# Kernel optimization log

Hardware: AMD Instinct MI355X
Metric: run time of the kernel (lower is better)

## Reference

```python
import jax, jax.numpy as jnp
import numpy as np
from jax import lax

B, N, C = 16, 2048, 128
NPOINT = 512
RADII = (0.1, 0.2, 0.4)
NSAMPLES = (16, 32, 48)
C_IN = C + 3          # use_xyz: relative xyz concatenated to features
C_OUT = 128
C_MID = C_OUT // 4    # mapping_func1 out channels (non-first-layer)


def fps(xyz, npoint):
    # sequential furthest point sampling; first index is 0 (matches CUDA FPS)
    b, n, _ = xyz.shape
    def step(carry, _):
        dist, last = carry
        p = xyz[jnp.arange(b), last]                    # (B,3) last selected point
        d = jnp.sum((xyz - p[:, None, :]) ** 2, -1)     # (B,N)
        dist = jnp.minimum(dist, d)
        nxt = jnp.argmax(dist, -1).astype(jnp.int32)
        return (dist, nxt), nxt
    idx0 = jnp.zeros((b,), jnp.int32)
    (_, _), rest = lax.scan(step, (jnp.full((b, n), 1e10, jnp.float32), idx0), None, length=npoint - 1)
    return jnp.concatenate([idx0[None], rest], 0).T     # (B,npoint)


def ball_query(xyz, new_xyz, radius, nsample):
    # first `nsample` in-ball indices (in original point order), pad with first hit
    n = xyz.shape[1]
    d2 = jnp.sum((new_xyz[:, :, None, :] - xyz[:, None, :, :]) ** 2, -1)  # (B,np,N)
    scores = jnp.where(d2 < radius * radius, jnp.arange(n, dtype=jnp.int32), n)
    vals = -lax.top_k(-scores, nsample)[0]               # ascending valid indices, invalid == n
    first = vals[..., :1]                                # center is always in its own ball
    return jnp.where(vals >= n, first, vals)             # (B,np,ns) int32


def gather_points(pts, idx):
    # pts (B,N,D), idx (B,np,ns) -> (B,np,ns,D)
    return jax.vmap(lambda p, i: p[i])(pts, idx)


def sa_forward(xyz, features, W1, b1, W2, b2, Wcr, bcr):
    fi = fps(xyz, NPOINT)
    new_xyz = jax.vmap(lambda p, i: p[i])(xyz, fi)       # (B,np,3)
    featT = jnp.transpose(features, (0, 2, 1))           # (B,N,C)
    outs = []
    for r, ns in zip(RADII, NSAMPLES):
        idx = ball_query(xyz, new_xyz, r, ns)
        g_xyz = gather_points(xyz, idx)                  # (B,np,ns,3) absolute neighbor coords
        rel = g_xyz - new_xyz[:, :, None, :]             # relative coords
        gf = gather_points(featT, idx)                   # (B,np,ns,C)
        x = jnp.concatenate([rel, gf], -1)               # (B,np,ns,C_in)
        dist = jnp.linalg.norm(rel, axis=-1, keepdims=True)
        ci = jnp.broadcast_to(new_xyz[:, :, None, :], g_xyz.shape)
        h10 = jnp.concatenate([dist, ci, g_xyz, rel], -1)        # relation prior (B,np,ns,10)
        h = jax.nn.relu(h10 @ W1 + b1) @ W2 + b2                 # dynamic weights (B,np,ns,C_in)
        pooled = jnp.max(jax.nn.relu(h * x), 2)                  # (B,np,C_in) max over neighbors
        outs.append(jax.nn.relu(pooled @ Wcr + bcr))             # channel raising (B,np,C_out)
    new_features = jnp.transpose(jnp.concatenate(outs, -1), (0, 2, 1))  # (B, 3*C_out, np)
    return new_xyz, new_features


def setup_inputs() -> dict:
    key = jax.random.key(0)
    ks = jax.random.split(key, 6)
    s = 0.05
    xyz = jax.random.uniform(ks[0], (B, N, 3), jnp.float32)
    features = jax.random.normal(ks[1], (B, C, N), jnp.float32)
    W1 = jax.random.normal(ks[2], (10, C_MID), jnp.float32) * s
    b1 = jnp.zeros((C_MID,), jnp.float32)
    W2 = jax.random.normal(ks[3], (C_MID, C_IN), jnp.float32) * s
    b2 = jnp.zeros((C_IN,), jnp.float32)
    Wcr = jax.random.normal(ks[4], (C_IN, C_OUT), jnp.float32) * s
    bcr = jnp.zeros((C_OUT,), jnp.float32)
    return dict(xyz=xyz, features=features, W1=W1, b1=b1, W2=W2, b2=b2, Wcr=Wcr, bcr=bcr)


def reference(xyz, features, W1, b1, W2, b2, Wcr, bcr):
    return sa_forward(xyz, features, W1, b1, W2, b2, Wcr, bcr)
```

## Files before the change

### kernel.cpp

```cpp
#include <hip/hip_runtime.h>
#include <hip/hip_bf16.h>

#define BATCH   16
#define NPTS    2048
#define NPOINT  512
#define CFEAT   128
#define CIN     131
#define CMID    32
#define NS_TOT  96
#define NTRANS  (BATCH * 256)
#define NCENT   (NPOINT * BATCH)
#define SMEM_BYTES 26688

typedef float v2f __attribute__((ext_vector_type(2)));

__device__ __forceinline__ float d2_rn(float ax, float ay, float az,
                                       float bx, float by, float bz) {
  float dx = __fsub_rn(ax, bx), dy = __fsub_rn(ay, by), dz = __fsub_rn(az, bz);
  return __fadd_rn(__fadd_rn(__fmul_rn(dx, dx), __fmul_rn(dy, dy)), __fmul_rn(dz, dz));
}

__device__ __forceinline__ unsigned long long wave_kmax64(unsigned long long k) {
#define KSTEP(CTRL, RMASK, BMASK)                                              \
  {                                                                            \
    unsigned hi = (unsigned)(k >> 32), lo = (unsigned)k;                       \
    unsigned thi = (unsigned)__builtin_amdgcn_update_dpp(                      \
        (int)hi, (int)hi, CTRL, RMASK, BMASK, false);                          \
    unsigned tlo = (unsigned)__builtin_amdgcn_update_dpp(                      \
        (int)lo, (int)lo, CTRL, RMASK, BMASK, false);                          \
    unsigned long long tk = ((unsigned long long)thi << 32) | tlo;             \
    k = tk > k ? tk : k;                                                       \
  }
  KSTEP(0x111, 0xf, 0xf)
  KSTEP(0x112, 0xf, 0xf)
  KSTEP(0x114, 0xf, 0xe)
  KSTEP(0x118, 0xf, 0xc)
  KSTEP(0x142, 0xa, 0xf)
  KSTEP(0x143, 0xc, 0xf)
#undef KSTEP
  return k;
}

__device__ __forceinline__ void fps_body(
    const float* __restrict__ xyz, float* __restrict__ out_xyz,
    int* prog, int b, int t, char* smem)
{
  __builtin_amdgcn_s_setprio(3);
  float* slx = (float*)smem;
  float* sly = (float*)(smem + 8192);
  float* slz = (float*)(smem + 16384);
  unsigned long long* skey = (unsigned long long*)(smem + 24576);
  int* slast = (int*)(smem + 24640);

  const float* xb = xyz + (size_t)b * NPTS * 3;
  for (int n = t; n < NPTS; n += 256) {
    const float* p = xb + n * 3;
    slx[n] = p[0]; sly[n] = p[1]; slz[n] = p[2];
  }
  if (t == 0) slast[0] = 0;
  __syncthreads();
  float lx[8], ly[8], lz[8], d[8];
#pragma unroll
  for (int i = 0; i < 8; ++i) {
    int n = (i << 8) + t;
    lx[i] = slx[n]; ly[i] = sly[n]; lz[i] = slz[n];
    d[i] = 1e10f;
  }
  int last = 0;
  int w = t >> 6;
  int tb = 0xFFF - t;
#pragma unroll 1
  for (int step = 1; step < NPOINT; ++step) {
    float pvx = slx[last], pvy = sly[last], pvz = slz[last];
    unsigned long long best = 0ull;
#pragma unroll
    for (int i = 0; i < 8; ++i) {
      float dd = d2_rn(lx[i], ly[i], lz[i], pvx, pvy, pvz);
      float nd = fminf(d[i], dd);
      d[i] = nd;
      unsigned long long k = ((unsigned long long)__float_as_uint(nd) << 32)
                           | (unsigned)(tb - (i << 8));
      best = (k > best) ? k : best;
    }
    unsigned long long wk = wave_kmax64(best);
    int par = step & 1;
    if ((t & 63) == 63) skey[par * 4 + w] = wk;
    __syncthreads();
    unsigned long long k0 = skey[par * 4 + 0], k1 = skey[par * 4 + 1];
    unsigned long long k2 = skey[par * 4 + 2], k3 = skey[par * 4 + 3];
    unsigned long long ka = k0 > k1 ? k0 : k1;
    unsigned long long kb = k2 > k3 ? k2 : k3;
    unsigned long long km = ka > kb ? ka : kb;
    last = (0xFFF - (int)((unsigned)km & 0xFFFu)) & (NPTS - 1);
    if (t == 0) slast[step] = last;
    if ((step & 7) == 7) {
      if (t < 24) {
        int k = t / 3, c = t - k * 3;
        int pt = slast[step - 7 + k];
        float v = (c == 0) ? slx[pt] : ((c == 1) ? sly[pt] : slz[pt]);
        out_xyz[((size_t)b * NPOINT + (step - 7 + k)) * 3 + c] = v;
      }
      if (prog && t == 0)
        __hip_atomic_store(prog + b, step + 1, __ATOMIC_RELEASE,
                           __HIP_MEMORY_SCOPE_AGENT);
    }
  }
}

__device__ __forceinline__ void transpose_body(
    const float* __restrict__ feat, float* __restrict__ featT,
    int* tdone, int m, int t, char* smem)
{
  float (*tile)[33] = (float (*)[33])smem;
  int b  = m >> 8;
  int c0 = ((m >> 6) & 3) << 5;
  int n0 = (m & 63) << 5;
  int tx = t & 31, ty = t >> 5;
  const float* src = feat  + (size_t)b * CFEAT * NPTS;
  float*       dst = featT + (size_t)b * NPTS * CFEAT;
#pragma unroll
  for (int i = 0; i < 4; ++i)
    tile[ty + 8 * i][tx] = src[(size_t)(c0 + ty + 8 * i) * NPTS + n0 + tx];
  __syncthreads();
#pragma unroll
  for (int i = 0; i < 4; ++i)
    dst[(size_t)(n0 + ty + 8 * i) * CFEAT + c0 + tx] = tile[tx][ty + 8 * i];
  if (tdone) {
    __syncthreads();
    if (t == 0)
      __hip_atomic_fetch_add(tdone + b, 1, __ATOMIC_RELEASE,
                             __HIP_MEMORY_SCOPE_AGENT);
  }
}

__device__ __forceinline__ void center_body(
    const float* __restrict__ xyz, const float* __restrict__ featT,
    const float* __restrict__ W1, const float* __restrict__ b1,
    const float* __restrict__ W2, const float* __restrict__ b2,
    const float* __restrict__ Wcr, const float* __restrict__ bcr,
    const float* __restrict__ new_xyz, float* __restrict__ out_feat,
    int* prog, int* tdone, int b, int j, int t, char* smem)
{
  int*   sIdx    = (int*)smem;
  float* sH1     = (float*)(smem + 384);
  float* sVr     = (float*)(smem + 14208);
  float* sPooled = (float*)(smem + 15744);
  float* sP      = (float*)(smem + 17328);

  if (prog) {
    if (t == 0) {
      int g = 0;
      while (__hip_atomic_load(prog + b, __ATOMIC_ACQUIRE,
                               __HIP_MEMORY_SCOPE_AGENT) <= j) {
        __builtin_amdgcn_s_sleep(8);
        if (++g > (1 << 20)) break;
      }
    }
    __syncthreads();
  }

  float cx = new_xyz[((size_t)b * NPOINT + j) * 3 + 0];
  float cy = new_xyz[((size_t)b * NPOINT + j) * 3 + 1];
  float cz = new_xyz[((size_t)b * NPOINT + j) * 3 + 2];

  {
    int w = t >> 6, lane = t & 63;
    const float* xb = xyz + (size_t)b * NPTS * 3;
    unsigned long long lt = (1ull << lane) - 1ull;
    if (w == 0) {
      int c0 = 0, c1 = 0;
      for (int it = 0; it < 32; ++it) {
        int n = (it << 6) + lane;
        float px = xb[n * 3 + 0], py = xb[n * 3 + 1], pz = xb[n * 3 + 2];
        float d2 = d2_rn(cx, cy, cz, px, py, pz);
        bool i0 = d2 < 0.01f, i1 = d2 < 0.04f;
        unsigned long long m0 = __ballot(i0), m1 = __ballot(i1);
        if (i0) { int pos = c0 + __popcll(m0 & lt); if (pos < 16) sIdx[pos] = n; }
        if (i1) { int pos = c1 + __popcll(m1 & lt); if (pos < 32) sIdx[16 + pos] = n; }
        c0 += __popcll(m0); c1 += __popcll(m1);
        if (c0 >= 16 && c1 >= 32) break;
      }
      int f0 = sIdx[0];
      int f1 = sIdx[16];
      if (lane >= c0 && lane < 16) sIdx[lane] = f0;
      if (lane >= c1 && lane < 32) sIdx[16 + lane] = f1;
    } else if (w == 1) {
      int c2 = 0;
      for (int it = 0; it < 32; ++it) {
        int n = (it << 6) + lane;
        float px = xb[n * 3 + 0], py = xb[n * 3 + 1], pz = xb[n * 3 + 2];
        float d2 = d2_rn(cx, cy, cz, px, py, pz);
        bool i2 = d2 < 0.16f;
        unsigned long long m2 = __ballot(i2);
        if (i2) { int pos = c2 + __popcll(m2 & lt); if (pos < 48) sIdx[48 + pos] = n; }
        c2 += __popcll(m2);
        if (c2 >= 48) break;
      }
      int f2 = sIdx[48];
      if (lane >= c2 && lane < 48) sIdx[48 + lane] = f2;
    }
  }
  __syncthreads();

  if (t < NS_TOT) {
    int idx = sIdx[t];
    const float* p = xyz + ((size_t)b * NPTS + (size_t)idx) * 3;
    float px = p[0], py = p[1], pz = p[2];
    float rx = __fsub_rn(px, cx), ry = __fsub_rn(py, cy), rz = __fsub_rn(pz, cz);
    float dist = sqrtf(__fadd_rn(__fadd_rn(__fmul_rn(rx, rx), __fmul_rn(ry, ry)),
                                 __fmul_rn(rz, rz)));
    float h10[10] = {dist, cx, cy, cz, px, py, pz, rx, ry, rz};
    float h1r[CMID];
#pragma unroll
    for (int m = 0; m < CMID / 2; ++m) {
      v2f a = { b1[2 * m], b1[2 * m + 1] };
#pragma unroll
      for (int i = 0; i < 10; ++i) {
        v2f wv = { W1[i * CMID + 2 * m], W1[i * CMID + 2 * m + 1] };
        v2f hv = { h10[i], h10[i] };
        a = __builtin_elementwise_fma(hv, wv, a);
      }
      v2f z = { 0.f, 0.f };
      a = __builtin_elementwise_max(a, z);
      h1r[2 * m] = a.x; h1r[2 * m + 1] = a.y;
    }
#pragma unroll
    for (int q = 0; q < 8; ++q)
      *(float4*)&sH1[t * 36 + 4 * q] = *(const float4*)&h1r[4 * q];
    v2f pa0 = { b2[0], 0.f }, pa1 = { b2[1], 0.f }, pa2 = { b2[2], 0.f };
#pragma unroll
    for (int m = 0; m < CMID / 2; ++m) {
      v2f hv = { h1r[2 * m], h1r[2 * m + 1] };
      v2f w0 = { W2[(2 * m) * CIN + 0], W2[(2 * m + 1) * CIN + 0] };
      v2f w1 = { W2[(2 * m) * CIN + 1], W2[(2 * m + 1) * CIN + 1] };
      v2f w2 = { W2[(2 * m) * CIN + 2], W2[(2 * m + 1) * CIN + 2] };
      pa0 = __builtin_elementwise_fma(hv, w0, pa0);
      pa1 = __builtin_elementwise_fma(hv, w1, pa1);
      pa2 = __builtin_elementwise_fma(hv, w2, pa2);
    }
    float a0 = __fadd_rn(pa0.x, pa0.y);
    float a1 = __fadd_rn(pa1.x, pa1.y);
    float a2 = __fadd_rn(pa2.x, pa2.y);
    sVr[t * 4 + 0] = fmaxf(__fmul_rn(a0, rx), 0.f);
    sVr[t * 4 + 1] = fmaxf(__fmul_rn(a1, ry), 0.f);
    sVr[t * 4 + 2] = fmaxf(__fmul_rn(a2, rz), 0.f);
  }
  if (prog) {
    if (t == 0) {
      int g = 0;
      while (__hip_atomic_load(tdone + b, __ATOMIC_ACQUIRE,
                               __HIP_MEMORY_SCOPE_AGENT) < 256) {
        __builtin_amdgcn_s_sleep(8);
        if (++g > (1 << 20)) break;
      }
    }
  }
  __syncthreads();

  {
    int w = t >> 6, lane = t & 63;
    v2f wA[16], wB[16];
#pragma unroll
    for (int m = 0; m < 16; ++m) {
      wA[m] = (v2f){ W2[(2 * m) * CIN + 3 + lane],
                     W2[(2 * m + 1) * CIN + 3 + lane] };
      wB[m] = (v2f){ W2[(2 * m) * CIN + 3 + lane + 64],
                     W2[(2 * m + 1) * CIN + 3 + lane + 64] };
    }
    float bA = b2[3 + lane], bB = b2[3 + lane + 64];
    const float* ftb = featT + (size_t)b * NPTS * CFEAT;
    int sBeg = w * 24, sEnd = sBeg + 24;
    float xA0 = ftb[(size_t)sIdx[sBeg] * CFEAT + lane];
    float xB0 = ftb[(size_t)sIdx[sBeg] * CFEAT + lane + 64];
    float xA1 = ftb[(size_t)sIdx[sBeg + 1] * CFEAT + lane];
    float xB1 = ftb[(size_t)sIdx[sBeg + 1] * CFEAT + lane + 64];
    float plA = 0.f, plB = 0.f;
#pragma unroll 1
    for (int s = sBeg; s < sEnd; ++s) {
      int sp2 = (s + 2 < sEnd) ? s + 2 : sEnd - 1;
      float xA2 = ftb[(size_t)sIdx[sp2] * CFEAT + lane];
      float xB2 = ftb[(size_t)sIdx[sp2] * CFEAT + lane + 64];
      const float4* h4 = (const float4*)&sH1[s * 36];
      v2f aAA = (v2f){ bA, 0.f }, aAB = (v2f){ 0.f, 0.f };
      v2f aBA = (v2f){ bB, 0.f }, aBB = (v2f){ 0.f, 0.f };
#pragma unroll
      for (int q = 0; q < 8; ++q) {
        float4 h = h4[q];
        v2f hxy = (v2f){ h.x, h.y }, hzw = (v2f){ h.z, h.w };
        aAA = __builtin_elementwise_fma(hxy, wA[2 * q],     aAA);
        aAB = __builtin_elementwise_fma(hzw, wA[2 * q + 1], aAB);
        aBA = __builtin_elementwise_fma(hxy, wB[2 * q],     aBA);
        aBB = __builtin_elementwise_fma(hzw, wB[2 * q + 1], aBB);
      }
      float hA = __fadd_rn(__fadd_rn(aAA.x, aAA.y), __fadd_rn(aAB.x, aAB.y));
      float hB = __fadd_rn(__fadd_rn(aBA.x, aBA.y), __fadd_rn(aBB.x, aBB.y));
      plA = fmaxf(plA, fmaxf(__fmul_rn(hA, xA0), 0.f));
      plB = fmaxf(plB, fmaxf(__fmul_rn(hB, xB0), 0.f));
      xA0 = xA1; xA1 = xA2; xB0 = xB1; xB1 = xB2;
      if (w == 0 && s == 15) {
        sPooled[0 * 132 + 3 + lane]      = plA;
        sPooled[0 * 132 + 3 + lane + 64] = plB;
        plA = 0.f; plB = 0.f;
      }
    }
    sP[w * 128 + lane]      = plA;
    sP[w * 128 + lane + 64] = plB;
  }
  if (t < 9) {
    int r = t / 3, c = t - r * 3;
    int s0 = (r == 0) ? 0 : (r == 1 ? 16 : 48);
    int s1 = (r == 0) ? 16 : (r == 1 ? 48 : 96);
    float pl = 0.f;
    for (int s = s0; s < s1; ++s) pl = fmaxf(pl, sVr[s * 4 + c]);
    sPooled[r * 132 + c] = pl;
  }
  __syncthreads();
  if (t < 128) {
    sPooled[1 * 132 + 3 + t] = fmaxf(sP[0 * 128 + t], sP[1 * 128 + t]);
    sPooled[2 * 132 + 3 + t] = fmaxf(sP[2 * 128 + t], sP[3 * 128 + t]);
  }
  __syncthreads();

  if (t < 128) {
    v2f s01 = { bcr[t], bcr[t] };
    float s2 = bcr[t];
#pragma unroll 1
    for (int k4 = 0; k4 < 128; k4 += 4) {
      float4 p0 = *(const float4*)&sPooled[k4];
      float4 p1 = *(const float4*)&sPooled[132 + k4];
      float4 p2 = *(const float4*)&sPooled[264 + k4];
#pragma unroll
      for (int u = 0; u < 4; ++u) {
        float w = Wcr[(k4 + u) * CFEAT + t];
        float e0 = (&p0.x)[u], e1 = (&p1.x)[u], e2 = (&p2.x)[u];
        s01 = __builtin_elementwise_fma((v2f){ e0, e1 }, (v2f){ w, w }, s01);
        s2  = fmaf(e2, w, s2);
      }
    }
#pragma unroll
    for (int k = 128; k < CIN; ++k) {
      float w = Wcr[k * CFEAT + t];
      s01 = __builtin_elementwise_fma((v2f){ sPooled[k], sPooled[132 + k] },
                                      (v2f){ w, w }, s01);
      s2  = fmaf(sPooled[264 + k], w, s2);
    }
    float* ob = out_feat + (size_t)b * 384 * NPOINT + j;
    ob[(size_t)(0 * CFEAT + t) * NPOINT] = fmaxf(s01.x, 0.f);
    ob[(size_t)(1 * CFEAT + t) * NPOINT] = fmaxf(s01.y, 0.f);
    ob[(size_t)(2 * CFEAT + t) * NPOINT] = fmaxf(s2, 0.f);
  }
}

__global__ __launch_bounds__(256) void fused_kernel(
    const float* __restrict__ xyz, const float* __restrict__ feat,
    const float* __restrict__ W1, const float* __restrict__ b1,
    const float* __restrict__ W2, const float* __restrict__ b2,
    const float* __restrict__ Wcr, const float* __restrict__ bcr,
    float* __restrict__ featT, float* __restrict__ out_xyz,
    float* __restrict__ out_feat, int* prog, int* tdone, int center_only)
{
  __shared__ __align__(16) char smem[SMEM_BYTES];
  int t = threadIdx.x;
  int id = blockIdx.x;
  if (!center_only) {
    if (id < BATCH) { fps_body(xyz, out_xyz, prog, id, t, smem); return; }
    if (id < BATCH + NTRANS) {
      transpose_body(feat, featT, tdone, id - BATCH, t, smem); return;
    }
    id -= BATCH + NTRANS;
  }
  int b = id & (BATCH - 1);
  int j = id >> 4;
  center_body(xyz, featT, W1, b1, W2, b2, Wcr, bcr, out_xyz, out_feat,
              prog, tdone, b, j, t, smem);
}

extern "C" void kernel_launch(void* const* d_in, const int* in_sizes, int n_in,
                              void* d_out, int out_size, void* d_ws, size_t ws_size,
                              hipStream_t stream) {
  const float* xyz  = (const float*)d_in[0];
  const float* feat = (const float*)d_in[1];
  const float* W1   = (const float*)d_in[2];
  const float* b1   = (const float*)d_in[3];
  const float* W2   = (const float*)d_in[4];
  const float* b2   = (const float*)d_in[5];
  const float* Wcr  = (const float*)d_in[6];
  const float* bcr  = (const float*)d_in[7];
  float* out_xyz  = (float*)d_out;
  float* out_feat = out_xyz + (size_t)BATCH * NPOINT * 3;
  float* featT    = (float*)d_ws;
  size_t featT_bytes = (size_t)BATCH * NPTS * CFEAT * sizeof(float);

  if (ws_size >= featT_bytes + 256) {
    int* flags = (int*)((char*)d_ws + featT_bytes);
    hipMemsetAsync(flags, 0, 128, stream);
    fused_kernel<<<BATCH + NTRANS + NCENT, 256, 0, stream>>>(
        xyz, feat, W1, b1, W2, b2, Wcr, bcr, featT, out_xyz, out_feat,
        flags, flags + 16, 0);
  } else {
    fused_kernel<<<BATCH + NTRANS, 256, 0, stream>>>(
        xyz, feat, W1, b1, W2, b2, Wcr, bcr, featT, out_xyz, out_feat,
        nullptr, nullptr, 0);
    fused_kernel<<<NCENT, 256, 0, stream>>>(
        xyz, feat, W1, b1, W2, b2, Wcr, bcr, featT, out_xyz, out_feat,
        nullptr, nullptr, 1);
  }
}
```

Measured before the change: 571.7 us.

## Run FPS in a single wave, stage outputs coalesced, then untranspose

```diff
diff --git a/kernel.cpp b/kernel.cpp
--- a/kernel.cpp
+++ b/kernel.cpp
@@ -49,8 +49,7 @@
   float* slx = (float*)smem;
   float* sly = (float*)(smem + 8192);
   float* slz = (float*)(smem + 16384);
-  unsigned long long* skey = (unsigned long long*)(smem + 24576);
-  int* slast = (int*)(smem + 24640);
+  int*   slast = (int*)(smem + 24576);
 
   const float* xb = xyz + (size_t)b * NPTS * 3;
   for (int n = t; n < NPTS; n += 256) {
@@ -59,46 +58,53 @@
   }
   if (t == 0) slast[0] = 0;
   __syncthreads();
-  float lx[8], ly[8], lz[8], d[8];
-#pragma unroll
-  for (int i = 0; i < 8; ++i) {
-    int n = (i << 8) + t;
-    lx[i] = slx[n]; ly[i] = sly[n]; lz[i] = slz[n];
-    d[i] = 1e10f;
-  }
-  int last = 0;
-  int w = t >> 6;
-  int tb = 0xFFF - t;
+  if (t >= 64) return;
+
+  v2f plx[16], ply[16], plz[16], dv[16];
+#pragma unroll
+  for (int k = 0; k < 16; ++k) {
+    int n0 = ((2 * k) << 6) + t, n1 = ((2 * k + 1) << 6) + t;
+    plx[k] = (v2f){ slx[n0], slx[n1] };
+    ply[k] = (v2f){ sly[n0], sly[n1] };
+    plz[k] = (v2f){ slz[n0], slz[n1] };
+    dv[k]  = (v2f){ 1e10f, 1e10f };
+  }
+  float pvx = slx[0], pvy = sly[0], pvz = slz[0];
+  unsigned tb = 0xFFFu - (unsigned)t;
 #pragma unroll 1
   for (int step = 1; step < NPOINT; ++step) {
-    float pvx = slx[last], pvy = sly[last], pvz = slz[last];
-    unsigned long long best = 0ull;
-#pragma unroll
-    for (int i = 0; i < 8; ++i) {
-      float dd = d2_rn(lx[i], ly[i], lz[i], pvx, pvy, pvz);
-      float nd = fminf(d[i], dd);
-      d[i] = nd;
-      unsigned long long k = ((unsigned long long)__float_as_uint(nd) << 32)
-                           | (unsigned)(tb - (i << 8));
-      best = (k > best) ? k : best;
-    }
+    unsigned bestu = 0u; unsigned bi = tb;
+    {
+#pragma clang fp contract(off)
+      v2f pvx2 = (v2f){ pvx, pvx };
+      v2f pvy2 = (v2f){ pvy, pvy };
+      v2f pvz2 = (v2f){ pvz, pvz };
+#pragma unroll
+      for (int k = 0; k < 16; ++k) {
+        v2f dx = plx[k] - pvx2;
+        v2f dy = ply[k] - pvy2;
+        v2f dz = plz[k] - pvz2;
+        v2f dd = dx * dx + dy * dy + dz * dz;
+        v2f nd = __builtin_elementwise_min(dv[k], dd);
+        dv[k] = nd;
+        unsigned u0 = __float_as_uint(nd.x);
+        unsigned u1 = __float_as_uint(nd.y);
+        if (u0 > bestu) { bestu = u0; bi = tb - (unsigned)((2 * k) << 6); }
+        if (u1 > bestu) { bestu = u1; bi = tb - (unsigned)((2 * k + 1) << 6); }
+      }
+    }
+    unsigned long long best = ((unsigned long long)bestu << 32) | bi;
     unsigned long long wk = wave_kmax64(best);
-    int par = step & 1;
-    if ((t & 63) == 63) skey[par * 4 + w] = wk;
-    __syncthreads();
-    unsigned long long k0 = skey[par * 4 + 0], k1 = skey[par * 4 + 1];
-    unsigned long long k2 = skey[par * 4 + 2], k3 = skey[par * 4 + 3];
-    unsigned long long ka = k0 > k1 ? k0 : k1;
-    unsigned long long kb = k2 > k3 ? k2 : k3;
-    unsigned long long km = ka > kb ? ka : kb;
-    last = (0xFFF - (int)((unsigned)km & 0xFFFu)) & (NPTS - 1);
+    unsigned lo63 = (unsigned)__builtin_amdgcn_readlane((int)(unsigned)wk, 63);
+    int last = (int)((0xFFFu - (lo63 & 0xFFFu)) & (NPTS - 1));
+    pvx = slx[last]; pvy = sly[last]; pvz = slz[last];
     if (t == 0) slast[step] = last;
-    if ((step & 7) == 7) {
-      if (t < 24) {
+    if ((step & 15) == 15) {
+      if (t < 48) {
         int k = t / 3, c = t - k * 3;
-        int pt = slast[step - 7 + k];
+        int pt = slast[step - 15 + k];
         float v = (c == 0) ? slx[pt] : ((c == 1) ? sly[pt] : slz[pt]);
-        out_xyz[((size_t)b * NPOINT + (step - 7 + k)) * 3 + c] = v;
+        out_xyz[((size_t)b * NPOINT + (step - 15 + k)) * 3 + c] = v;
       }
       if (prog && t == 0)
         __hip_atomic_store(prog + b, step + 1, __ATOMIC_RELEASE,
@@ -139,7 +145,8 @@
     const float* __restrict__ W2, const float* __restrict__ b2,
     const float* __restrict__ Wcr, const float* __restrict__ bcr,
     const float* __restrict__ new_xyz, float* __restrict__ out_feat,
-    int* prog, int* tdone, int b, int j, int t, char* smem)
+    float* __restrict__ out_tmp, int* prog, int* tdone,
+    int b, int j, int t, char* smem)
 {
   int*   sIdx    = (int*)smem;
   float* sH1     = (float*)(smem + 384);
@@ -324,7 +331,7 @@
   if (t < 128) {
     v2f s01 = { bcr[t], bcr[t] };
     float s2 = bcr[t];
-#pragma unroll 1
+#pragma unroll 2
     for (int k4 = 0; k4 < 128; k4 += 4) {
       float4 p0 = *(const float4*)&sPooled[k4];
       float4 p1 = *(const float4*)&sPooled[132 + k4];
@@ -344,10 +351,17 @@
                                       (v2f){ w, w }, s01);
       s2  = fmaf(sPooled[264 + k], w, s2);
     }
-    float* ob = out_feat + (size_t)b * 384 * NPOINT + j;
-    ob[(size_t)(0 * CFEAT + t) * NPOINT] = fmaxf(s01.x, 0.f);
-    ob[(size_t)(1 * CFEAT + t) * NPOINT] = fmaxf(s01.y, 0.f);
-    ob[(size_t)(2 * CFEAT + t) * NPOINT] = fmaxf(s2, 0.f);
+    if (out_tmp) {
+      float* ob = out_tmp + ((size_t)b * NPOINT + j) * 384;
+      ob[t]       = fmaxf(s01.x, 0.f);
+      ob[128 + t] = fmaxf(s01.y, 0.f);
+      ob[256 + t] = fmaxf(s2, 0.f);
+    } else {
+      float* ob = out_feat + (size_t)b * 384 * NPOINT + j;
+      ob[(size_t)(0 * CFEAT + t) * NPOINT] = fmaxf(s01.x, 0.f);
+      ob[(size_t)(1 * CFEAT + t) * NPOINT] = fmaxf(s01.y, 0.f);
+      ob[(size_t)(2 * CFEAT + t) * NPOINT] = fmaxf(s2, 0.f);
+    }
   }
 }
 
@@ -357,7 +371,8 @@
     const float* __restrict__ W2, const float* __restrict__ b2,
     const float* __restrict__ Wcr, const float* __restrict__ bcr,
     float* __restrict__ featT, float* __restrict__ out_xyz,
-    float* __restrict__ out_feat, int* prog, int* tdone, int center_only)
+    float* __restrict__ out_feat, float* __restrict__ out_tmp,
+    int* prog, int* tdone, int center_only)
 {
   __shared__ __align__(16) char smem[SMEM_BYTES];
   int t = threadIdx.x;
@@ -372,7 +387,24 @@
   int b = id & (BATCH - 1);
   int j = id >> 4;
   center_body(xyz, featT, W1, b1, W2, b2, Wcr, bcr, out_xyz, out_feat,
-              prog, tdone, b, j, t, smem);
+              out_tmp, prog, tdone, b, j, t, smem);
+}
+
+__global__ __launch_bounds__(256) void untranspose_kernel(
+    const float* __restrict__ tmp, float* __restrict__ out_feat)
+{
+  __shared__ float tile[32][33];
+  int jt = blockIdx.x, ct = blockIdx.y, b = blockIdx.z;
+  int t = threadIdx.x, tx = t & 31, ty = t >> 5;
+  const float* src = tmp      + (size_t)b * NPOINT * 384;
+  float*       dst = out_feat + (size_t)b * 384 * NPOINT;
+#pragma unroll
+  for (int i = 0; i < 4; ++i)
+    tile[ty + 8 * i][tx] = src[(size_t)(jt * 32 + ty + 8 * i) * 384 + ct * 32 + tx];
+  __syncthreads();
+#pragma unroll
+  for (int i = 0; i < 4; ++i)
+    dst[(size_t)(ct * 32 + ty + 8 * i) * NPOINT + jt * 32 + tx] = tile[tx][ty + 8 * i];
 }
 
 extern "C" void kernel_launch(void* const* d_in, const int* in_sizes, int n_in,
@@ -390,19 +422,23 @@
   float* out_feat = out_xyz + (size_t)BATCH * NPOINT * 3;
   float* featT    = (float*)d_ws;
   size_t featT_bytes = (size_t)BATCH * NPTS * CFEAT * sizeof(float);
-
-  if (ws_size >= featT_bytes + 256) {
-    int* flags = (int*)((char*)d_ws + featT_bytes);
+  size_t tmp_bytes   = (size_t)BATCH * NPOINT * 384 * sizeof(float);
+
+  if (ws_size >= featT_bytes + tmp_bytes + 256) {
+    float* tmp = (float*)((char*)d_ws + featT_bytes);
+    int* flags = (int*)((char*)d_ws + featT_bytes + tmp_bytes);
     hipMemsetAsync(flags, 0, 128, stream);
     fused_kernel<<<BATCH + NTRANS + NCENT, 256, 0, stream>>>(
         xyz, feat, W1, b1, W2, b2, Wcr, bcr, featT, out_xyz, out_feat,
-        flags, flags + 16, 0);
+        tmp, flags, flags + 16, 0);
+    untranspose_kernel<<<dim3(NPOINT / 32, 384 / 32, BATCH), 256, 0, stream>>>(
+        tmp, out_feat);
   } else {
     fused_kernel<<<BATCH + NTRANS, 256, 0, stream>>>(
         xyz, feat, W1, b1, W2, b2, Wcr, bcr, featT, out_xyz, out_feat,
-        nullptr, nullptr, 0);
+        nullptr, nullptr, nullptr, 0);
     fused_kernel<<<NCENT, 256, 0, stream>>>(
         xyz, feat, W1, b1, W2, b2, Wcr, bcr, featT, out_xyz, out_feat,
-        nullptr, nullptr, 1);
-  }
-}
+        nullptr, nullptr, nullptr, 1);
+  }
+}
```

Result: slower. 667.5 us (+16.8%).
